# Performance work log

Hardware: AMD Instinct MI355X
Metric: run time of the kernel (lower is better)

Reference implementation:

```python
import jax, jax.numpy as jnp
import numpy as np

N_NODES = 5000
N_EDGES = 40000
NUM_ATOM_TYPES = 100
HID = 32            # multiplicity of 0e and 1o in irreps_hidden
EDGE_ATTR_DIM = 8
NUM_BOND_TYPES = 5
OUT_SCALARS = 2 * 6 + 1  # max_charge=6 -> 13x0e
CUTOFF = 5.0
SQRT3 = 1.7320508075688772


def _sh(edge_vec):
    # o3.SphericalHarmonics('1x0e + 1x1o', normalize=True, normalization='component')
    d = jnp.sqrt(jnp.sum(edge_vec * edge_vec, axis=-1) + 1e-12)
    n = edge_vec / d[:, None]
    sh0 = jnp.ones(edge_vec.shape[0], edge_vec.dtype)          # [E]
    sh1 = SQRT3 * n[:, (1, 2, 0)]                              # [E,3], e3nn (y,z,x) order
    return sh0, sh1, d


def _soft_one_hot(d):
    # e3nn.math.soft_one_hot_linspace(d, 0, cutoff, 8, basis='gaussian', cutoff=True)
    values = jnp.linspace(0.0, CUTOFF, EDGE_ATTR_DIM + 2)[1:-1]
    step = CUTOFF / (EDGE_ATTR_DIM + 1)
    diff = (d[:, None] - values[None, :]) / step
    return jnp.exp(-diff * diff) / 1.12


def _mlp(x, W0, b0, W1, b1):
    # ScalarMLP(in, out, hidden=[in], SiLU)
    return jax.nn.silu(x @ W0 + b0) @ W1 + b1


def _tp_init(s, sh0, sh1, w):
    # FCTP(32x0e, 1x0e+1x1o -> 32x0e+32x1o); paths: 0e*0e->0e, 0e*1o->1o
    E = s.shape[0]
    w1 = w[:, : HID * HID].reshape(E, HID, HID)
    w2 = w[:, HID * HID :].reshape(E, HID, HID)
    c = 1.0 / np.sqrt(HID)  # fan-in = 32 per output irrep
    out_s = c * jnp.einsum('eu,euw->ew', s * sh0[:, None], w1)
    out_v = c * jnp.einsum('eu,ei,euw->ewi', s, sh1, w2)
    return out_s, out_v


def _tp_hidden(s, v, sh0, sh1, w):
    # FCTP(32x0e+32x1o, 1x0e+1x1o -> 32x0e+32x1o)
    # path order: 0e*0e->0e, 0e*1o->1o, 1o*0e->1o, 1o*1o->0e
    E = s.shape[0]
    ws = w.reshape(E, 4, HID, HID)
    c = 1.0 / np.sqrt(2 * HID)  # fan-in = 64 per output irrep
    dot = jnp.einsum('eui,ei->eu', v, sh1) / SQRT3  # CG(1,1->0) = delta/sqrt(3)
    out_s = c * (jnp.einsum('eu,euw->ew', s * sh0[:, None], ws[:, 0]) +
                 jnp.einsum('eu,euw->ew', dot, ws[:, 3]))
    out_v = c * (jnp.einsum('eu,ei,euw->ewi', s, sh1, ws[:, 1]) +
                 jnp.einsum('eui,euw->ewi', v * sh0[:, None, None], ws[:, 2]))
    return out_s, out_v


def _edge_tp(s1, v1, s2, v2, sh0, sh1, w):
    # FCTP(64x0e+64x1o (concat of two hidden), 1x0e+1x1o -> 5x0e)
    # blocks in concat order: s_src, v_src, s_dst, v_dst
    E = s1.shape[0]
    ws = w.reshape(E, 4, HID, NUM_BOND_TYPES)
    c = 1.0 / np.sqrt(4 * HID)  # fan-in = 128
    d1 = jnp.einsum('eui,ei->eu', v1, sh1) / SQRT3
    d2 = jnp.einsum('eui,ei->eu', v2, sh1) / SQRT3
    return c * (jnp.einsum('eu,euw->ew', s1 * sh0[:, None], ws[:, 0]) +
                jnp.einsum('eu,euw->ew', d1, ws[:, 1]) +
                jnp.einsum('eu,euw->ew', s2 * sh0[:, None], ws[:, 2]) +
                jnp.einsum('eu,euw->ew', d2, ws[:, 3]))


def _scatter_mean(ms, mv, dst, n):
    cnt = jax.ops.segment_sum(jnp.ones(dst.shape[0], ms.dtype), dst, num_segments=n)
    cnt = jnp.maximum(cnt, 1.0)
    s = jax.ops.segment_sum(ms, dst, num_segments=n) / cnt[:, None]
    v = jax.ops.segment_sum(mv, dst, num_segments=n) / cnt[:, None, None]
    return s, v


def setup_inputs() -> dict:
    key = jax.random.key(0)
    ks = jax.random.split(key, 16)
    def w(k, shape, fan_in):
        return jax.random.normal(k, shape, dtype=jnp.float32) / np.sqrt(fan_in)
    inp = {}
    inp['coordinates'] = jax.random.normal(ks[0], (N_NODES, 3), dtype=jnp.float32) * 1.5
    inp['atom_types'] = jax.random.randint(ks[1], (N_NODES,), 0, NUM_ATOM_TYPES)
    inp['edge_index'] = jax.random.randint(ks[2], (2, N_EDGES), 0, N_NODES)
    inp['atom_embed'] = jax.random.normal(ks[3], (NUM_ATOM_TYPES, HID), dtype=jnp.float32)
    inp['ip_W0'] = w(ks[4], (EDGE_ATTR_DIM, EDGE_ATTR_DIM), EDGE_ATTR_DIM)
    inp['ip_b0'] = jnp.zeros((EDGE_ATTR_DIM,), jnp.float32)
    inp['ip_W1'] = w(ks[5], (EDGE_ATTR_DIM, 2 * HID * HID), EDGE_ATTR_DIM)
    inp['ip_b1'] = jnp.zeros((2 * HID * HID,), jnp.float32)
    inp['ly_W0'] = w(ks[6], (EDGE_ATTR_DIM, EDGE_ATTR_DIM), EDGE_ATTR_DIM)
    inp['ly_b0'] = jnp.zeros((EDGE_ATTR_DIM,), jnp.float32)
    inp['ly_W1'] = w(ks[7], (EDGE_ATTR_DIM, 4 * HID * HID), EDGE_ATTR_DIM)
    inp['ly_b1'] = jnp.zeros((4 * HID * HID,), jnp.float32)
    inp['ly_Ws'] = jax.random.normal(ks[8], (HID, HID), dtype=jnp.float32)
    inp['ly_Wv'] = jax.random.normal(ks[9], (HID, HID), dtype=jnp.float32)
    inp['et_W0'] = w(ks[10], (EDGE_ATTR_DIM, EDGE_ATTR_DIM), EDGE_ATTR_DIM)
    inp['et_b0'] = jnp.zeros((EDGE_ATTR_DIM,), jnp.float32)
    inp['et_W1'] = w(ks[11], (EDGE_ATTR_DIM, 4 * HID * NUM_BOND_TYPES), EDGE_ATTR_DIM)
    inp['et_b1'] = jnp.zeros((4 * HID * NUM_BOND_TYPES,), jnp.float32)
    inp['no_W1'] = jax.random.normal(ks[12], (HID, OUT_SCALARS), dtype=jnp.float32)
    inp['no_W2'] = jax.random.normal(ks[13], (OUT_SCALARS, OUT_SCALARS), dtype=jnp.float32)
    return inp


def reference(coordinates, atom_types, edge_index, atom_embed,
              ip_W0, ip_b0, ip_W1, ip_b1,
              ly_W0, ly_b0, ly_W1, ly_b1, ly_Ws, ly_Wv,
              et_W0, et_b0, et_W1, et_b1, no_W1, no_W2):
    n = coordinates.shape[0]
    src, dst = edge_index[0], edge_index[1]
    edge_vec = coordinates[dst] - coordinates[src]
    sh0, sh1, d = _sh(edge_vec)
    edge_attr = _soft_one_hot(d)                              # [E,8]
    # initial projector: Conv(32x0e -> 32x0e+32x1o)
    s0 = atom_embed[atom_types]                               # [N,32]
    w_ip = _mlp(edge_attr, ip_W0, ip_b0, ip_W1, ip_b1)        # [E,2048]
    ms, mv = _tp_init(s0[src], sh0, sh1, w_ip)
    s, v = _scatter_mean(ms, mv, dst, n)                      # [N,32],[N,32,3]
    # one LinearSelfInteraction(Conv) layer
    w_ly = _mlp(edge_attr, ly_W0, ly_b0, ly_W1, ly_b1)        # [E,4096]
    ms, mv = _tp_hidden(s[src], v[src], sh0, sh1, w_ly)
    cs, cv = _scatter_mean(ms, mv, dst, n)
    lc = 1.0 / np.sqrt(HID)  # e3nn o3.Linear normalization
    s = cs + lc * (s @ ly_Ws)
    v = cv + lc * jnp.einsum('eui,uw->ewi', v, ly_Wv)
    # edge output: FCTP([h_src, h_dst], edge_sh) with radial weights
    w_et = _mlp(edge_attr, et_W0, et_b0, et_W1, et_b1)        # [E,640]
    edge_out = _edge_tp(s[src], v[src], s[dst], v[dst], sh0, sh1, w_et)  # [E,5]
    # node output MLP on detached scalar channel (13x0e)
    sd = jax.lax.stop_gradient(s)
    h = jax.nn.silu(sd @ no_W1 / np.sqrt(HID))
    node_out = h @ no_W2 / np.sqrt(OUT_SCALARS)               # [N,13]
    return edge_out, node_out
```

## Files before the change

kernel.cpp:

```cpp
#include <hip/hip_runtime.h>

#define NN 5000
#define NE 40000

typedef unsigned int u32;
typedef unsigned short u16;
typedef __fp16 h16x2 __attribute__((ext_vector_type(2)));
typedef _Float16 f16x8 __attribute__((ext_vector_type(8)));
typedef __attribute__((ext_vector_type(4))) float f32x4;

union AF { u32 u[4]; f16x8 v; uint4 q; };

__device__ __forceinline__ float siluf(float x) { return x / (1.f + __expf(-x)); }

__device__ __forceinline__ u32 f2bf_u(float f) {
  u32 x = __float_as_uint(f);
  return (x + 0x7FFFu + ((x >> 16) & 1u)) >> 16;
}
__device__ __forceinline__ u32 packbf2(float lo, float hi) {
  return f2bf_u(lo) | (f2bf_u(hi) << 16);
}
__device__ __forceinline__ u32 pkh2(float a, float b) {
  union { h16x2 h; u32 u; } r;
  r.h = __builtin_amdgcn_cvt_pkrtz(a, b);
  return r.u;
}
__device__ __forceinline__ u16 f2h(float v) {
  _Float16 h = (_Float16)v;
  return *(u16*)&h;
}
__device__ __forceinline__ void unpack8(uint4 q, float* f) {
  f[0] = __uint_as_float(q.x << 16); f[1] = __uint_as_float(q.x & 0xFFFF0000u);
  f[2] = __uint_as_float(q.y << 16); f[3] = __uint_as_float(q.y & 0xFFFF0000u);
  f[4] = __uint_as_float(q.z << 16); f[5] = __uint_as_float(q.z & 0xFFFF0000u);
  f[6] = __uint_as_float(q.w << 16); f[7] = __uint_as_float(q.w & 0xFFFF0000u);
}
__device__ __forceinline__ float dot8f(const float* h, const float* w, float init) {
  float a = init;
#pragma unroll
  for (int k = 0; k < 8; k++) a = fmaf(h[k], w[k], a);
  return a;
}
__device__ __forceinline__ void mlp8(const float* ea, const float* __restrict__ W0,
                                     const float* __restrict__ b0, float* h) {
#pragma unroll
  for (int j = 0; j < 8; j++) {
    float a = b0[j];
#pragma unroll
    for (int i = 0; i < 8; i++) a += ea[i] * W0[i*8 + j];
    h[j] = siluf(a);
  }
}
__device__ __forceinline__ AF mkfrag(float hs, const float* s) {
  AF a;
  a.u[0] = pkh2(hs*s[0], hs*s[1]);
  a.u[1] = pkh2(hs*s[2], hs*s[3]);
  a.u[2] = pkh2(hs*s[4], hs*s[5]);
  a.u[3] = pkh2(hs*s[6], hs*s[7]);
  return a;
}
__device__ __forceinline__ float bf2f(u16 v) { return __uint_as_float(((u32)v) << 16); }

__global__ __launch_bounds__(256) void k_prep(
    const float* __restrict__ ipW1, const float* __restrict__ ipb1,
    const float* __restrict__ lyW1, const float* __restrict__ lyb1,
    u16* __restrict__ ipT, u16* __restrict__ lyT) {
  int b = blockIdx.x;
  if (b < 16) {
    int h = b >> 3;
    int t0 = (b & 7)*2304 + threadIdx.x*9;
#pragma unroll
    for (int j = 0; j < 9; j++) {
      int t = t0 + j;
      int kch = t >> 9, rem = t & 511;
      int col = rem >> 3, kk = rem & 7;
      int k = kch*8 + kk;
      int basec = (h == 0) ? ((col >> 5)*1024 + (col & 31))
                           : ((col < 32) ? (2048 + col) : (3072 + (col - 32)));
      float v = (k < 256) ? lyW1[(k >> 5)*4096 + basec + (k & 31)*32]
                          : lyb1[basec + (k - 256)*32];
      lyT[h*18432 + t] = f2h(v);
    }
  } else {
    int t0 = (b - 16)*2304 + threadIdx.x*9;
#pragma unroll
    for (int j = 0; j < 9; j++) {
      int t = t0 + j;
      int kch = t >> 9, rem = t & 511;
      int col = rem >> 3, kk = rem & 7;
      int k = kch*8 + kk;
      int pth = col >> 5, w = col & 31;
      float v = (k < 256) ? ipW1[(k >> 5)*2048 + pth*1024 + (k & 31)*32 + w]
                          : ipb1[pth*1024 + (k - 256)*32 + w];
      ipT[t] = f2h(v);
    }
  }
}

__global__ __launch_bounds__(256) void k_conv1(
    const float* __restrict__ coords, const int* __restrict__ eidx,
    const float* __restrict__ emb, const int* __restrict__ atype,
    const float* __restrict__ ipW0, const float* __restrict__ ipb0,
    const float* __restrict__ lyW0, const float* __restrict__ lyb0,
    const float* __restrict__ etW0, const float* __restrict__ etb0,
    const u16* __restrict__ ipT,
    float* __restrict__ sh, float* __restrict__ h_ly, float* __restrict__ h_et,
    int* __restrict__ cur, int* __restrict__ slot, u16* __restrict__ msg) {
  int wid = threadIdx.x >> 6, lane = threadIdx.x & 63;
  int tile = blockIdx.x*4 + wid;
  int m = lane & 15, q = lane >> 4;
  int e = tile*16 + m;
  int s = eidx[e], d = eidx[NE + e];
  float vx = coords[d*3+0] - coords[s*3+0];
  float vy = coords[d*3+1] - coords[s*3+1];
  float vz = coords[d*3+2] - coords[s*3+2];
  float dist = sqrtf(vx*vx + vy*vy + vz*vz + 1e-12f);
  float dinv = 1.f / dist;
  const float SQ3 = 1.7320508075688772f;
  float sh0 = SQ3 * vy * dinv;
  float sh1 = SQ3 * vz * dinv;
  float sh2 = SQ3 * vx * dinv;
  int srow = atype[s];
  float ea[8];
  const float step = 5.f / 9.f;
#pragma unroll
  for (int jj = 0; jj < 8; jj++) {
    float diff = (dist - step * (float)(jj+1)) * (9.f / 5.f);
    ea[jj] = __expf(-diff*diff) * (1.f / 1.12f);
  }
  float hip[8], hly[8], het[8];
  mlp8(ea, ipW0, ipb0, hip);
  mlp8(ea, lyW0, lyb0, hly);
  mlp8(ea, etW0, etb0, het);
  int t = 0;
  if (q == 0) {
    sh[e*3+0] = sh0; sh[e*3+1] = sh1; sh[e*3+2] = sh2;
    { float4 f0 = {hly[0],hly[1],hly[2],hly[3]}, f1 = {hly[4],hly[5],hly[6],hly[7]};
      *(float4*)&h_ly[e*8] = f0; *(float4*)&h_ly[e*8+4] = f1; }
    { float4 f0 = {het[0],het[1],het[2],het[3]}, f1 = {het[4],het[5],het[6],het[7]};
      *(float4*)&h_et[e*8] = f0; *(float4*)&h_et[e*8+4] = f1; }
    int* cp = &cur[d];
    atomicCAS(cp, (int)0xAAAAAAAA, 0);
    t = atomicAdd(cp, 1);
    slot[e] = t;
  }
  float4 sA = *(const float4*)&emb[srow*32 + q*8];
  float4 sB = *(const float4*)&emb[srow*32 + q*8 + 4];
  float sf[8] = {sA.x,sA.y,sA.z,sA.w,sB.x,sB.y,sB.z,sB.w};
  f32x4 acc0 = {0.f,0.f,0.f,0.f}, acc1 = acc0, acc2 = acc0, acc3 = acc0;
  const float cs = 0.17677669529663687f;
#pragma unroll
  for (int ks = 0; ks < 9; ks++) {
    float hs = (ks < 8) ? hip[ks] : 1.f;
    AF a = mkfrag(hs, sf);
    int c2 = (ks*4 + q)*64;
    AF b0, b1f, b2, b3;
    b0.q  = *(const uint4*)&ipT[(c2 +  0 + m)*8];
    b1f.q = *(const uint4*)&ipT[(c2 + 16 + m)*8];
    b2.q  = *(const uint4*)&ipT[(c2 + 32 + m)*8];
    b3.q  = *(const uint4*)&ipT[(c2 + 48 + m)*8];
    acc0 = __builtin_amdgcn_mfma_f32_16x16x32_f16(a.v, b0.v,  acc0, 0, 0, 0);
    acc1 = __builtin_amdgcn_mfma_f32_16x16x32_f16(a.v, b1f.v, acc1, 0, 0, 0);
    acc2 = __builtin_amdgcn_mfma_f32_16x16x32_f16(a.v, b2.v,  acc2, 0, 0, 0);
    acc3 = __builtin_amdgcn_mfma_f32_16x16x32_f16(a.v, b3.v,  acc3, 0, 0, 0);
  }
#pragma unroll
  for (int r = 0; r < 4; r++) {
    int L = q*4 + r;
    int tE = __shfl(t, L, 64);
    int dn = __shfl(d, L, 64);
    float s0v = __shfl(sh0, L, 64);
    float s1v = __shfl(sh1, L, 64);
    float s2v = __shfl(sh2, L, 64);
    if (tE < 64) {
      u16* mp = msg + ((size_t)dn*64 + tE)*128;
      float m0 = cs*acc2[r], m1 = cs*acc3[r];
      uint2 p0 = { packbf2(cs*acc0[r], m0*s0v), packbf2(m0*s1v, m0*s2v) };
      *(uint2*)&mp[m*4] = p0;
      uint2 p1 = { packbf2(cs*acc1[r], m1*s0v), packbf2(m1*s1v, m1*s2v) };
      *(uint2*)&mp[64 + m*4] = p1;
    }
  }
}

__global__ __launch_bounds__(256) void k_gather1(
    const u16* __restrict__ msg, const int* __restrict__ cur,
    float* __restrict__ s1, float* __restrict__ v1soa) {
  int ln = threadIdx.x >> 7, c = threadIdx.x & 127;
  int n = blockIdx.x*2 + ln;
  int deg = min(cur[n], 64);
  const u16* base = msg + (size_t)n*64*128 + c;
  float acc = 0.f;
  int j = 0;
  for (; j + 4 <= deg; j += 4) {
    float x0 = bf2f(base[(j+0)*128]);
    float x1 = bf2f(base[(j+1)*128]);
    float x2 = bf2f(base[(j+2)*128]);
    float x3 = bf2f(base[(j+3)*128]);
    acc += (x0 + x1) + (x2 + x3);
  }
  for (; j < deg; j++) acc += bf2f(base[j*128]);
  acc /= (float)max(deg, 1);
  int col = c >> 2, comp = c & 3;
  if (comp == 0) s1[n*32 + col] = acc;
  else           v1soa[(comp-1)*160000 + n*32 + col] = acc;
}

__global__ __launch_bounds__(256) void k_conv2(
    const float* __restrict__ hE, const float* __restrict__ sh,
    const float* __restrict__ s1, const float* __restrict__ v1soa,
    const int* __restrict__ eidx, const int* __restrict__ slot,
    const u16* __restrict__ lyT,
    u16* __restrict__ msgA, u16* __restrict__ msgB) {
  int wid = threadIdx.x >> 6, lane = threadIdx.x & 63;
  const bool scalarHalf = blockIdx.x < 625;
  int blk = scalarHalf ? blockIdx.x : blockIdx.x - 625;
  int tile = blk*4 + wid;
  int m = lane & 15, q = lane >> 4;
  const u16* Bg = lyT + (scalarHalf ? 0 : 18432);
  const float c = 0.125f;
  int e = tile*16 + m;
  int srcn = eidx[e];
  int dnv  = eidx[NE + e];
  int slv  = slot[e];
  float s0p = sh[e*3+0], s1p = sh[e*3+1], s2p = sh[e*3+2];
  float4 hA = *(const float4*)&hE[e*8];
  float4 hB = *(const float4*)&hE[e*8 + 4];
  float hf[8] = {hA.x,hA.y,hA.z,hA.w,hB.x,hB.y,hB.z,hB.w};

  if (scalarHalf) {
    float4 sA = *(const float4*)&s1[srcn*32 + q*8];
    float4 sB = *(const float4*)&s1[srcn*32 + q*8 + 4];
    float sf[8] = {sA.x,sA.y,sA.z,sA.w,sB.x,sB.y,sB.z,sB.w};
    f32x4 acc0 = {0.f,0.f,0.f,0.f}, acc1 = acc0, acc2 = acc0, acc3 = acc0;
#pragma unroll
    for (int ks = 0; ks < 9; ks++) {
      float hs = (ks < 8) ? hf[ks] : 1.f;
      AF a = mkfrag(hs, sf);
      int c2 = (ks*4 + q)*64;
      AF b0, b1f, b2, b3;
      b0.q  = *(const uint4*)&Bg[(c2 +  0 + m)*8];
      b1f.q = *(const uint4*)&Bg[(c2 + 16 + m)*8];
      b2.q  = *(const uint4*)&Bg[(c2 + 32 + m)*8];
      b3.q  = *(const uint4*)&Bg[(c2 + 48 + m)*8];
      acc0 = __builtin_amdgcn_mfma_f32_16x16x32_f16(a.v, b0.v,  acc0, 0, 0, 0);
      acc1 = __builtin_amdgcn_mfma_f32_16x16x32_f16(a.v, b1f.v, acc1, 0, 0, 0);
      acc2 = __builtin_amdgcn_mfma_f32_16x16x32_f16(a.v, b2.v,  acc2, 0, 0, 0);
      acc3 = __builtin_amdgcn_mfma_f32_16x16x32_f16(a.v, b3.v,  acc3, 0, 0, 0);
    }
#pragma unroll
    for (int r = 0; r < 4; r++) {
      int L = q*4 + r;
      int tE = __shfl(slv, L, 64);
      int dn = __shfl(dnv, L, 64);
      float s0v = __shfl(s0p, L, 64);
      float s1v = __shfl(s1p, L, 64);
      float s2v = __shfl(s2p, L, 64);
      if (tE < 64) {
        u16* mp = msgA + ((size_t)dn*64 + tE)*128;
        float m0 = c*acc2[r], m1 = c*acc3[r];
        uint2 p0 = { packbf2(c*acc0[r], m0*s0v), packbf2(m0*s1v, m0*s2v) };
        *(uint2*)&mp[m*4] = p0;
        uint2 p1 = { packbf2(c*acc1[r], m1*s0v), packbf2(m1*s1v, m1*s2v) };
        *(uint2*)&mp[64 + m*4] = p1;
      }
    }
  } else {
    const float is3 = 0.5773502691896258f;
    float vf[3][8];
#pragma unroll
    for (int i = 0; i < 3; i++) {
      float4 aa = *(const float4*)&v1soa[i*160000 + srcn*32 + q*8];
      float4 bb = *(const float4*)&v1soa[i*160000 + srcn*32 + q*8 + 4];
      vf[i][0]=aa.x; vf[i][1]=aa.y; vf[i][2]=aa.z; vf[i][3]=aa.w;
      vf[i][4]=bb.x; vf[i][5]=bb.y; vf[i][6]=bb.z; vf[i][7]=bb.w;
    }
    float df[8];
#pragma unroll
    for (int j = 0; j < 8; j++)
      df[j] = (vf[0][j]*s0p + vf[1][j]*s1p + vf[2][j]*s2p) * is3;
    f32x4 z = {0.f,0.f,0.f,0.f};
    f32x4 aV00 = z, aV01 = z, aV10 = z, aV11 = z, aV20 = z, aV21 = z, aD0 = z, aD1 = z;
#pragma unroll
    for (int ks = 0; ks < 9; ks++) {
      float hs = (ks < 8) ? hf[ks] : 1.f;
      int c2 = (ks*4 + q)*64;
      AF b0, b1f, b2, b3;
      b0.q  = *(const uint4*)&Bg[(c2 +  0 + m)*8];
      b1f.q = *(const uint4*)&Bg[(c2 + 16 + m)*8];
      b2.q  = *(const uint4*)&Bg[(c2 + 32 + m)*8];
      b3.q  = *(const uint4*)&Bg[(c2 + 48 + m)*8];
      AF a0 = mkfrag(hs, vf[0]);
      AF a1 = mkfrag(hs, vf[1]);
      AF a2 = mkfrag(hs, vf[2]);
      AF ad = mkfrag(hs, df);
      aV00 = __builtin_amdgcn_mfma_f32_16x16x32_f16(a0.v, b0.v,  aV00, 0, 0, 0);
      aV01 = __builtin_amdgcn_mfma_f32_16x16x32_f16(a0.v, b1f.v, aV01, 0, 0, 0);
      aV10 = __builtin_amdgcn_mfma_f32_16x16x32_f16(a1.v, b0.v,  aV10, 0, 0, 0);
      aV11 = __builtin_amdgcn_mfma_f32_16x16x32_f16(a1.v, b1f.v, aV11, 0, 0, 0);
      aV20 = __builtin_amdgcn_mfma_f32_16x16x32_f16(a2.v, b0.v,  aV20, 0, 0, 0);
      aV21 = __builtin_amdgcn_mfma_f32_16x16x32_f16(a2.v, b1f.v, aV21, 0, 0, 0);
      aD0  = __builtin_amdgcn_mfma_f32_16x16x32_f16(ad.v, b2.v,  aD0,  0, 0, 0);
      aD1  = __builtin_amdgcn_mfma_f32_16x16x32_f16(ad.v, b3.v,  aD1,  0, 0, 0);
    }
#pragma unroll
    for (int r = 0; r < 4; r++) {
      int L = q*4 + r;
      int tE = __shfl(slv, L, 64);
      int dn = __shfl(dnv, L, 64);
      if (tE < 64) {
        u16* mp = msgB + ((size_t)dn*64 + tE)*128;
        uint2 p0 = { packbf2(c*aD0[r], c*aV00[r]), packbf2(c*aV10[r], c*aV20[r]) };
        *(uint2*)&mp[m*4] = p0;
        uint2 p1 = { packbf2(c*aD1[r], c*aV01[r]), packbf2(c*aV11[r], c*aV21[r]) };
        *(uint2*)&mp[64 + m*4] = p1;
      }
    }
  }
}

__global__ __launch_bounds__(256) void k_gather2(
    const u16* __restrict__ msgA, const u16* __restrict__ msgB,
    const int* __restrict__ cur,
    const float* __restrict__ s1, const float* __restrict__ v1soa,
    const float* __restrict__ Ws, const float* __restrict__ Wv,
    const float* __restrict__ noW1, const float* __restrict__ noW2,
    float* __restrict__ s2, float* __restrict__ v2, float* __restrict__ outN) {
  __shared__ float sb[2][32];
  __shared__ float hb[2][13];
  int ln = threadIdx.x >> 7, c = threadIdx.x & 127;
  int n = blockIdx.x*2 + ln;
  int deg = min(cur[n], 64);
  const u16* bA = msgA + (size_t)n*64*128 + c;
  const u16* bB = msgB + (size_t)n*64*128 + c;
  float acc = 0.f;
  int j = 0;
  for (; j + 4 <= deg; j += 4) {
    float x0 = bf2f(bA[(j+0)*128]) + bf2f(bB[(j+0)*128]);
    float x1 = bf2f(bA[(j+1)*128]) + bf2f(bB[(j+1)*128]);
    float x2 = bf2f(bA[(j+2)*128]) + bf2f(bB[(j+2)*128]);
    float x3 = bf2f(bA[(j+3)*128]) + bf2f(bB[(j+3)*128]);
    acc += (x0 + x1) + (x2 + x3);
  }
  for (; j < deg; j++) acc += bf2f(bA[j*128]) + bf2f(bB[j*128]);
  acc /= (float)max(deg, 1);
  const float lc = 0.17677669529663687f;
  int col = c >> 2, comp = c & 3;
  if (comp == 0) {
    float ss = 0.f;
#pragma unroll 8
    for (int u = 0; u < 32; u++) ss += s1[n*32 + u] * Ws[u*32 + col];
    float val = acc + lc*ss;
    s2[n*32 + col] = val;
    sb[ln][col] = val;
  } else {
    int i = comp - 1;
    float sv = 0.f;
#pragma unroll 8
    for (int u = 0; u < 32; u++) sv += v1soa[i*160000 + n*32 + u] * Wv[u*32 + col];
    v2[n*96 + col*3 + i] = acc + lc*sv;
  }
  __syncthreads();
  const float i32 = 0.17677669529663687f;
  if (c < 13) {
    float a = 0.f;
#pragma unroll 8
    for (int u = 0; u < 32; u++) a += sb[ln][u] * noW1[u*13 + c];
    hb[ln][c] = siluf(a * i32);
  }
  __syncthreads();
  const float i13 = 0.2773500981126146f;
  if (c < 13) {
    float a = 0.f;
#pragma unroll
    for (int j2 = 0; j2 < 13; j2++) a += hb[ln][j2] * noW2[j2*13 + c];
    outN[n*13 + c] = a * i13;
  }
}

__global__ __launch_bounds__(256) void k_e3(
    const float* __restrict__ hE, const float* __restrict__ sh,
    const float* __restrict__ s2, const float* __restrict__ v2,
    const int* __restrict__ eidx,
    const float* __restrict__ W1, const float* __restrict__ b1,
    float* __restrict__ out) {
  __shared__ uint4 WQ[640];
  __shared__ float BQ[640];
  for (int t = threadIdx.x; t < 640; t += 256) {
    int u = t & 31, pw = t >> 5, p2 = pw / 5, w = pw - p2*5;
    int col = p2*160 + u*5 + w;
    const float* s = W1 + col;
    uint4 q;
    q.x = packbf2(s[0],      s[640]);
    q.y = packbf2(s[1280],   s[1920]);
    q.z = packbf2(s[2560],   s[3200]);
    q.w = packbf2(s[3840],   s[4480]);
    WQ[t] = q;
    BQ[t] = b1[col];
  }
  __syncthreads();
  const int g = threadIdx.x >> 5, tw = threadIdx.x & 31;
  const float c = 0.08838834764831845f;
  const float is3 = 0.5773502691896258f;
  for (int p = blockIdx.x*8 + g; p*2 < NE; p += gridDim.x*8) {
    int e0 = p*2, e1 = e0 + 1;
    float h0[8], h1[8];
    {
      float4 qa = *(const float4*)&hE[e0*8];
      float4 qb = *(const float4*)&hE[e0*8+4];
      h0[0]=qa.x; h0[1]=qa.y; h0[2]=qa.z; h0[3]=qa.w;
      h0[4]=qb.x; h0[5]=qb.y; h0[6]=qb.z; h0[7]=qb.w;
      float4 qc = *(const float4*)&hE[e1*8];
      float4 qd = *(const float4*)&hE[e1*8+4];
      h1[0]=qc.x; h1[1]=qc.y; h1[2]=qc.z; h1[3]=qc.w;
      h1[4]=qd.x; h1[5]=qd.y; h1[6]=qd.z; h1[7]=qd.w;
    }
    int sA = eidx[e0], dA = eidx[NE+e0];
    int sB = eidx[e1], dB = eidx[NE+e1];
    float sa0 = sh[e0*3+0], sa1 = sh[e0*3+1], sa2 = sh[e0*3+2];
    float sb0 = sh[e1*3+0], sb1 = sh[e1*3+1], sb2 = sh[e1*3+2];
    float c00 = s2[sA*32 + tw];
    float c01 = (v2[sA*96+tw*3+0]*sa0 + v2[sA*96+tw*3+1]*sa1 + v2[sA*96+tw*3+2]*sa2) * is3;
    float c02 = s2[dA*32 + tw];
    float c03 = (v2[dA*96+tw*3+0]*sa0 + v2[dA*96+tw*3+1]*sa1 + v2[dA*96+tw*3+2]*sa2) * is3;
    float c10 = s2[sB*32 + tw];
    float c11 = (v2[sB*96+tw*3+0]*sb0 + v2[sB*96+tw*3+1]*sb1 + v2[sB*96+tw*3+2]*sb2) * is3;
    float c12 = s2[dB*32 + tw];
    float c13 = (v2[dB*96+tw*3+0]*sb0 + v2[dB*96+tw*3+1]*sb1 + v2[dB*96+tw*3+2]*sb2) * is3;
    float part0[5] = {0,0,0,0,0};
    float part1[5] = {0,0,0,0,0};
#pragma unroll
    for (int pp = 0; pp < 4; pp++) {
      float cp0 = (pp==0) ? c00 : (pp==1) ? c01 : (pp==2) ? c02 : c03;
      float cp1 = (pp==0) ? c10 : (pp==1) ? c11 : (pp==2) ? c12 : c13;
#pragma unroll
      for (int w = 0; w < 5; w++) {
        int idx = (pp*5 + w)*32 + tw;
        float f[8];
        unpack8(WQ[idx], f);
        float bv = BQ[idx];
        part0[w] = fmaf(cp0, dot8f(h0, f, bv), part0[w]);
        part1[w] = fmaf(cp1, dot8f(h1, f, bv), part1[w]);
      }
    }
#pragma unroll
    for (int off = 16; off > 0; off >>= 1)
#pragma unroll
      for (int w = 0; w < 5; w++) {
        part0[w] += __shfl_xor(part0[w], off, 32);
        part1[w] += __shfl_xor(part1[w], off, 32);
      }
    float outv = 0.f;
#pragma unroll
    for (int w = 0; w < 5; w++) {
      if (tw == w)     outv = part0[w];
      if (tw == 5 + w) outv = part1[w];
    }
    if (tw < 10) out[e0*5 + tw] = c * outv;
  }
}

extern "C" void kernel_launch(void* const* d_in, const int* in_sizes, int n_in,
                              void* d_out, int out_size, void* d_ws, size_t ws_size,
                              hipStream_t stream) {
  (void)in_sizes; (void)n_in; (void)out_size; (void)ws_size;
  const float* coords = (const float*)d_in[0];
  const int*   atype  = (const int*)d_in[1];
  const int*   eidx   = (const int*)d_in[2];
  const float* emb    = (const float*)d_in[3];
  const float* ipW0 = (const float*)d_in[4];
  const float* ipb0 = (const float*)d_in[5];
  const float* ipW1 = (const float*)d_in[6];
  const float* ipb1 = (const float*)d_in[7];
  const float* lyW0 = (const float*)d_in[8];
  const float* lyb0 = (const float*)d_in[9];
  const float* lyW1 = (const float*)d_in[10];
  const float* lyb1 = (const float*)d_in[11];
  const float* lyWs = (const float*)d_in[12];
  const float* lyWv = (const float*)d_in[13];
  const float* etW0 = (const float*)d_in[14];
  const float* etb0 = (const float*)d_in[15];
  const float* etW1 = (const float*)d_in[16];
  const float* etb1 = (const float*)d_in[17];
  const float* noW1 = (const float*)d_in[18];
  const float* noW2 = (const float*)d_in[19];

  float* ws = (float*)d_ws;
  float* sh    = ws;
  float* h_ly  = ws + 120000;
  float* h_et  = ws + 440000;
  float* s1    = ws + 760000;
  float* v1soa = ws + 920000;
  float* s2    = ws + 1400000;
  float* v2    = ws + 1560000;
  int*   cur   = (int*)(ws + 2040000);
  int*   slot  = (int*)(ws + 2045000);
  u16*   msgA  = (u16*)(ws + 2085000);
  u16*   msgB  = (u16*)(ws + 22565000);
  u16*   lyT   = (u16*)(ws + 43045000);
  u16*   ipT   = (u16*)(ws + 43063432);

  float* outE = (float*)d_out;
  float* outN = (float*)d_out + NE*5;

  k_prep<<<24, 256, 0, stream>>>(ipW1, ipb1, lyW1, lyb1, ipT, lyT);
  k_conv1<<<625, 256, 0, stream>>>(coords, eidx, emb, atype,
                                   ipW0, ipb0, lyW0, lyb0, etW0, etb0,
                                   ipT, sh, h_ly, h_et, cur, slot, msgA);
  k_gather1<<<NN/2, 256, 0, stream>>>(msgA, cur, s1, v1soa);
  k_conv2<<<1250, 256, 0, stream>>>(h_ly, sh, s1, v1soa, eidx, slot,
                                    lyT, msgA, msgB);
  k_gather2<<<NN/2, 256, 0, stream>>>(msgA, msgB, cur, s1, v1soa,
                                      lyWs, lyWv, noW1, noW2, s2, v2, outN);
  k_e3<<<1024, 256, 0, stream>>>(h_et, sh, s2, v2, eidx, etW1, etb1, outE);
}
```

Before: 168.1 us.

## Fuse first gather into conv2 and gather2, removing k_gather1 launch

Drops the separate gather kernel for the first convolution. Each edge in conv2 now re-reduces its source node's message bucket (up to 64 bf16 rows) to get the mean s1/v1 on the fly, and gather2 recomputes the same reduction for the self-interaction term. Message buffers are split into msg1, msg2A and msg2B so the first-layer messages are not overwritten. This removes one launch and the s1/v1 round trip, but it adds redundant reads: every edge rereads a whole neighbour bucket, which is about 8x more traffic into conv2.

```diff
diff --git a/kernel.cpp b/kernel.cpp
--- a/kernel.cpp
+++ b/kernel.cpp
@@ -105,7 +105,7 @@
     const float* __restrict__ etW0, const float* __restrict__ etb0,
     const u16* __restrict__ ipT,
     float* __restrict__ sh, float* __restrict__ h_ly, float* __restrict__ h_et,
-    int* __restrict__ cur, int* __restrict__ slot, u16* __restrict__ msg) {
+    int* __restrict__ cur, int* __restrict__ slot, u16* __restrict__ msg1) {
   int wid = threadIdx.x >> 6, lane = threadIdx.x & 63;
   int tile = blockIdx.x*4 + wid;
   int m = lane & 15, q = lane >> 4;
@@ -173,7 +173,7 @@
     float s1v = __shfl(sh1, L, 64);
     float s2v = __shfl(sh2, L, 64);
     if (tE < 64) {
-      u16* mp = msg + ((size_t)dn*64 + tE)*128;
+      u16* mp = msg1 + ((size_t)dn*64 + tE)*128;
       float m0 = cs*acc2[r], m1 = cs*acc3[r];
       uint2 p0 = { packbf2(cs*acc0[r], m0*s0v), packbf2(m0*s1v, m0*s2v) };
       *(uint2*)&mp[m*4] = p0;
@@ -183,34 +183,11 @@
   }
 }
 
-__global__ __launch_bounds__(256) void k_gather1(
-    const u16* __restrict__ msg, const int* __restrict__ cur,
-    float* __restrict__ s1, float* __restrict__ v1soa) {
-  int ln = threadIdx.x >> 7, c = threadIdx.x & 127;
-  int n = blockIdx.x*2 + ln;
-  int deg = min(cur[n], 64);
-  const u16* base = msg + (size_t)n*64*128 + c;
-  float acc = 0.f;
-  int j = 0;
-  for (; j + 4 <= deg; j += 4) {
-    float x0 = bf2f(base[(j+0)*128]);
-    float x1 = bf2f(base[(j+1)*128]);
-    float x2 = bf2f(base[(j+2)*128]);
-    float x3 = bf2f(base[(j+3)*128]);
-    acc += (x0 + x1) + (x2 + x3);
-  }
-  for (; j < deg; j++) acc += bf2f(base[j*128]);
-  acc /= (float)max(deg, 1);
-  int col = c >> 2, comp = c & 3;
-  if (comp == 0) s1[n*32 + col] = acc;
-  else           v1soa[(comp-1)*160000 + n*32 + col] = acc;
-}
-
 __global__ __launch_bounds__(256) void k_conv2(
     const float* __restrict__ hE, const float* __restrict__ sh,
-    const float* __restrict__ s1, const float* __restrict__ v1soa,
     const int* __restrict__ eidx, const int* __restrict__ slot,
-    const u16* __restrict__ lyT,
+    const int* __restrict__ cur,
+    const u16* __restrict__ msg1, const u16* __restrict__ lyT,
     u16* __restrict__ msgA, u16* __restrict__ msgB) {
   int wid = threadIdx.x >> 6, lane = threadIdx.x & 63;
   const bool scalarHalf = blockIdx.x < 625;
@@ -228,10 +205,33 @@
   float4 hB = *(const float4*)&hE[e*8 + 4];
   float hf[8] = {hA.x,hA.y,hA.z,hA.w,hB.x,hB.y,hB.z,hB.w};
 
+  int dg = min(cur[srcn], 64);
+  float inv = 1.f / (float)max(dg, 1);
+  float sfa[8], v0a[8], v1a[8], v2a[8];
+#pragma unroll
+  for (int i = 0; i < 8; i++) { sfa[i]=0.f; v0a[i]=0.f; v1a[i]=0.f; v2a[i]=0.f; }
+  const u16* bkt = msg1 + (size_t)srcn*8192 + q*32;
+  for (int j = 0; j < dg; j++) {
+    const uint4* rp = (const uint4*)(bkt + (size_t)j*128);
+#pragma unroll
+    for (int k2 = 0; k2 < 4; k2++) {
+      uint4 X = rp[k2];
+      int c0 = k2*2;
+      sfa[c0]   += __uint_as_float(X.x << 16);
+      v0a[c0]   += __uint_as_float(X.x & 0xFFFF0000u);
+      v1a[c0]   += __uint_as_float(X.y << 16);
+      v2a[c0]   += __uint_as_float(X.y & 0xFFFF0000u);
+      sfa[c0+1] += __uint_as_float(X.z << 16);
+      v0a[c0+1] += __uint_as_float(X.z & 0xFFFF0000u);
+      v1a[c0+1] += __uint_as_float(X.w << 16);
+      v2a[c0+1] += __uint_as_float(X.w & 0xFFFF0000u);
+    }
+  }
+
   if (scalarHalf) {
-    float4 sA = *(const float4*)&s1[srcn*32 + q*8];
-    float4 sB = *(const float4*)&s1[srcn*32 + q*8 + 4];
-    float sf[8] = {sA.x,sA.y,sA.z,sA.w,sB.x,sB.y,sB.z,sB.w};
+    float sf[8];
+#pragma unroll
+    for (int i = 0; i < 8; i++) sf[i] = sfa[i] * inv;
     f32x4 acc0 = {0.f,0.f,0.f,0.f}, acc1 = acc0, acc2 = acc0, acc3 = acc0;
 #pragma unroll
     for (int ks = 0; ks < 9; ks++) {
@@ -269,11 +269,10 @@
     const float is3 = 0.5773502691896258f;
     float vf[3][8];
 #pragma unroll
-    for (int i = 0; i < 3; i++) {
-      float4 aa = *(const float4*)&v1soa[i*160000 + srcn*32 + q*8];
-      float4 bb = *(const float4*)&v1soa[i*160000 + srcn*32 + q*8 + 4];
-      vf[i][0]=aa.x; vf[i][1]=aa.y; vf[i][2]=aa.z; vf[i][3]=aa.w;
-      vf[i][4]=bb.x; vf[i][5]=bb.y; vf[i][6]=bb.z; vf[i][7]=bb.w;
+    for (int i = 0; i < 8; i++) {
+      vf[0][i] = v0a[i] * inv;
+      vf[1][i] = v1a[i] * inv;
+      vf[2][i] = v2a[i] * inv;
     }
     float df[8];
 #pragma unroll
@@ -320,45 +319,58 @@
 }
 
 __global__ __launch_bounds__(256) void k_gather2(
+    const u16* __restrict__ msg1,
     const u16* __restrict__ msgA, const u16* __restrict__ msgB,
     const int* __restrict__ cur,
-    const float* __restrict__ s1, const float* __restrict__ v1soa,
     const float* __restrict__ Ws, const float* __restrict__ Wv,
     const float* __restrict__ noW1, const float* __restrict__ noW2,
     float* __restrict__ s2, float* __restrict__ v2, float* __restrict__ outN) {
+  __shared__ float sA[2][32];
+  __shared__ float vA[2][3][32];
   __shared__ float sb[2][32];
   __shared__ float hb[2][13];
   int ln = threadIdx.x >> 7, c = threadIdx.x & 127;
   int n = blockIdx.x*2 + ln;
   int deg = min(cur[n], 64);
-  const u16* bA = msgA + (size_t)n*64*128 + c;
-  const u16* bB = msgB + (size_t)n*64*128 + c;
-  float acc = 0.f;
+  const u16* b1p = msg1 + (size_t)n*8192 + c;
+  const u16* bAp = msgA + (size_t)n*8192 + c;
+  const u16* bBp = msgB + (size_t)n*8192 + c;
+  float a1 = 0.f, a2 = 0.f;
   int j = 0;
   for (; j + 4 <= deg; j += 4) {
-    float x0 = bf2f(bA[(j+0)*128]) + bf2f(bB[(j+0)*128]);
-    float x1 = bf2f(bA[(j+1)*128]) + bf2f(bB[(j+1)*128]);
-    float x2 = bf2f(bA[(j+2)*128]) + bf2f(bB[(j+2)*128]);
-    float x3 = bf2f(bA[(j+3)*128]) + bf2f(bB[(j+3)*128]);
-    acc += (x0 + x1) + (x2 + x3);
-  }
-  for (; j < deg; j++) acc += bf2f(bA[j*128]) + bf2f(bB[j*128]);
-  acc /= (float)max(deg, 1);
+    float y0 = bf2f(b1p[(j+0)*128]), y1 = bf2f(b1p[(j+1)*128]);
+    float y2 = bf2f(b1p[(j+2)*128]), y3 = bf2f(b1p[(j+3)*128]);
+    a1 += (y0 + y1) + (y2 + y3);
+    float x0 = bf2f(bAp[(j+0)*128]) + bf2f(bBp[(j+0)*128]);
+    float x1 = bf2f(bAp[(j+1)*128]) + bf2f(bBp[(j+1)*128]);
+    float x2 = bf2f(bAp[(j+2)*128]) + bf2f(bBp[(j+2)*128]);
+    float x3 = bf2f(bAp[(j+3)*128]) + bf2f(bBp[(j+3)*128]);
+    a2 += (x0 + x1) + (x2 + x3);
+  }
+  for (; j < deg; j++) {
+    a1 += bf2f(b1p[j*128]);
+    a2 += bf2f(bAp[j*128]) + bf2f(bBp[j*128]);
+  }
+  float inv = 1.f / (float)max(deg, 1);
+  a1 *= inv; a2 *= inv;
+  int col = c >> 2, comp = c & 3;
+  if (comp == 0) sA[ln][col] = a1;
+  else           vA[ln][comp-1][col] = a1;
+  __syncthreads();
   const float lc = 0.17677669529663687f;
-  int col = c >> 2, comp = c & 3;
   if (comp == 0) {
     float ss = 0.f;
 #pragma unroll 8
-    for (int u = 0; u < 32; u++) ss += s1[n*32 + u] * Ws[u*32 + col];
-    float val = acc + lc*ss;
+    for (int u = 0; u < 32; u++) ss += sA[ln][u] * Ws[u*32 + col];
+    float val = a2 + lc*ss;
     s2[n*32 + col] = val;
     sb[ln][col] = val;
   } else {
     int i = comp - 1;
     float sv = 0.f;
 #pragma unroll 8
-    for (int u = 0; u < 32; u++) sv += v1soa[i*160000 + n*32 + u] * Wv[u*32 + col];
-    v2[n*96 + col*3 + i] = acc + lc*sv;
+    for (int u = 0; u < 32; u++) sv += vA[ln][i][u] * Wv[u*32 + col];
+    v2[n*96 + col*3 + i] = a2 + lc*sv;
   }
   __syncthreads();
   const float i32 = 0.17677669529663687f;
@@ -489,16 +501,15 @@
   float* sh    = ws;
   float* h_ly  = ws + 120000;
   float* h_et  = ws + 440000;
-  float* s1    = ws + 760000;
-  float* v1soa = ws + 920000;
-  float* s2    = ws + 1400000;
-  float* v2    = ws + 1560000;
-  int*   cur   = (int*)(ws + 2040000);
-  int*   slot  = (int*)(ws + 2045000);
-  u16*   msgA  = (u16*)(ws + 2085000);
-  u16*   msgB  = (u16*)(ws + 22565000);
-  u16*   lyT   = (u16*)(ws + 43045000);
-  u16*   ipT   = (u16*)(ws + 43063432);
+  float* s2    = ws + 760000;
+  float* v2    = ws + 920000;
+  int*   cur   = (int*)(ws + 1400000);
+  int*   slot  = (int*)(ws + 1405000);
+  u16*   lyT   = (u16*)(ws + 1445000);
+  u16*   ipT   = (u16*)(ws + 1463432);
+  u16*   msg1  = (u16*)(ws + 1480000);
+  u16*   msg2A = (u16*)(ws + 21960000);
+  u16*   msg2B = (u16*)(ws + 42440000);
 
   float* outE = (float*)d_out;
   float* outN = (float*)d_out + NE*5;
@@ -506,11 +517,10 @@
   k_prep<<<24, 256, 0, stream>>>(ipW1, ipb1, lyW1, lyb1, ipT, lyT);
   k_conv1<<<625, 256, 0, stream>>>(coords, eidx, emb, atype,
                                    ipW0, ipb0, lyW0, lyb0, etW0, etb0,
-                                   ipT, sh, h_ly, h_et, cur, slot, msgA);
-  k_gather1<<<NN/2, 256, 0, stream>>>(msgA, cur, s1, v1soa);
-  k_conv2<<<1250, 256, 0, stream>>>(h_ly, sh, s1, v1soa, eidx, slot,
-                                    lyT, msgA, msgB);
-  k_gather2<<<NN/2, 256, 0, stream>>>(msgA, msgB, cur, s1, v1soa,
+                                   ipT, sh, h_ly, h_et, cur, slot, msg1);
+  k_conv2<<<1250, 256, 0, stream>>>(h_ly, sh, eidx, slot, cur,
+                                    msg1, lyT, msg2A, msg2B);
+  k_gather2<<<NN/2, 256, 0, stream>>>(msg1, msg2A, msg2B, cur,
                                       lyWs, lyWv, noW1, noW2, s2, v2, outN);
   k_e3<<<1024, 256, 0, stream>>>(h_et, sh, s2, v2, eidx, etW1, etb1, outE);
 }
```

Result: slower. 178.2 us (+6.0%).
